# Performance work log

Hardware: AMD Instinct MI355X
Metric: run time of the kernel (lower is better)

The kernel has to match this reference:

```python
import math
import jax, jax.numpy as jnp
import numpy as np

D_MODEL = 1024
N_HEADS = 16
D_FF = 4096
B = 4
T = 1024  # tgt len
S = 1024  # src len
EPS = 1e-6


def _linear_params(key, d_in, d_out):
    kw, kb = jax.random.split(key)
    w = jax.random.normal(kw, (d_out, d_in), dtype=jnp.float32) * 0.02
    b = jax.random.normal(kb, (d_out,), dtype=jnp.float32) * 0.02
    return w, b


def setup_inputs() -> dict:
    key = jax.random.key(0)
    ks = jax.random.split(key, 16)
    x = jax.random.normal(ks[0], (B, T, D_MODEL), dtype=jnp.float32)
    memory = jax.random.normal(ks[1], (B, S, D_MODEL), dtype=jnp.float32)
    # causal [B, T, T] mask (dim==3 branch) and padding [B, S] mask (dim==2 branch)
    tgt_mask = jnp.broadcast_to(jnp.tril(jnp.ones((T, T), dtype=jnp.int32)), (B, T, T))
    src_mask = jnp.ones((B, S), dtype=jnp.int32)
    inp = {"x": x, "memory": memory, "tgt_mask": tgt_mask, "src_mask": src_mask}
    names = ["sa_wq", "sa_wk", "sa_wv", "sa_wo", "ca_wq", "ca_wk", "ca_wv", "ca_wo"]
    for i, n in enumerate(names):
        w, b = _linear_params(ks[2 + i], D_MODEL, D_MODEL)
        inp[n] = w
        inp[n.replace("w", "b")] = b
    inp["ff_w1"], inp["ff_b1"] = _linear_params(ks[10], D_MODEL, D_FF)
    inp["ff_w2"], inp["ff_b2"] = _linear_params(ks[11], D_FF, D_MODEL)
    for i, n in enumerate(["ln1", "ln2", "ln3"]):
        inp[n + "_w"] = jnp.ones((D_MODEL,), dtype=jnp.float32)
        inp[n + "_b"] = jnp.zeros((D_MODEL,), dtype=jnp.float32)
    return inp


def layernorm(x, w, b):
    # torch-faithful: unbiased std (N-1), eps added to std (not variance)
    mean = jnp.mean(x, axis=-1, keepdims=True)
    d = x - mean
    std = jnp.sqrt(jnp.sum(d * d, axis=-1, keepdims=True) / (x.shape[-1] - 1))
    return w * d / (std + EPS) + b


def mha(q_in, kv_in, mask, wq, bq, wk, bk, wv, bv, wo, bo):
    Bb, Tq, D = q_in.shape
    Tk = kv_in.shape[1]
    dk = D // N_HEADS
    if mask.ndim == 2:
        mask4 = mask[:, None, None, :]
    else:
        mask4 = mask[:, None, :, :]
    q = (q_in @ wq.T + bq).reshape(Bb, Tq, N_HEADS, dk).transpose(0, 2, 1, 3)
    k = (kv_in @ wk.T + bk).reshape(Bb, Tk, N_HEADS, dk).transpose(0, 2, 1, 3)
    v = (kv_in @ wv.T + bv).reshape(Bb, Tk, N_HEADS, dk).transpose(0, 2, 1, 3)
    scores = jnp.einsum("bhqd,bhkd->bhqk", q, k) / math.sqrt(dk)
    scores = jnp.where(mask4 == 0, jnp.float32(-1e9), scores)
    attn = jax.nn.softmax(scores, axis=-1)
    out = jnp.einsum("bhqk,bhkd->bhqd", attn, v)
    out = out.transpose(0, 2, 1, 3).reshape(Bb, Tq, D)
    return out @ wo.T + bo


def reference(x, memory, tgt_mask, src_mask,
              sa_wq, sa_bq, sa_wk, sa_bk, sa_wv, sa_bv, sa_wo, sa_bo,
              ca_wq, ca_bq, ca_wk, ca_bk, ca_wv, ca_bv, ca_wo, ca_bo,
              ff_w1, ff_b1, ff_w2, ff_b2,
              ln1_w, ln1_b, ln2_w, ln2_b, ln3_w, ln3_b):
    # pre-norm decoder block (norm_first=True), dropout=0 (eval)
    h = layernorm(x, ln1_w, ln1_b)
    x = x + mha(h, h, tgt_mask, sa_wq, sa_bq, sa_wk, sa_bk, sa_wv, sa_bv, sa_wo, sa_bo)
    h = layernorm(x, ln2_w, ln2_b)
    x = x + mha(h, memory, src_mask, ca_wq, ca_bq, ca_wk, ca_bk, ca_wv, ca_bv, ca_wo, ca_bo)
    h = layernorm(x, ln3_w, ln3_b)
    x = x + (jax.nn.relu(h @ ff_w1.T + ff_b1) @ ff_w2.T + ff_b2)
    return x
```

## Files before the change

kernel.cpp:

```cpp
#include <hip/hip_runtime.h>
#include <hip/hip_bf16.h>

typedef unsigned short u16;
typedef __attribute__((ext_vector_type(4))) float f32x4;
typedef __attribute__((ext_vector_type(8))) short s16x8;
typedef __attribute__((ext_vector_type(4))) short s16x4;
typedef __attribute__((ext_vector_type(8))) __bf16 bf16x8;

#define NTOK 4096
#define DMODEL 1024
#define DFF 4096
#define NH 16
#define TSEQ 1024


__device__ __forceinline__ u16 f2b_hw(float f) {
  union { __bf16 h; u16 u; } cv;
  cv.h = (__bf16)f;
  return cv.u;
}

__device__ __forceinline__ f32x4 mfma16(s16x8 a, s16x8 b, f32x4 c) {
  return __builtin_amdgcn_mfma_f32_16x16x32_bf16((bf16x8)a, (bf16x8)b, c, 0, 0, 0);
}

__device__ __forceinline__ void gload16(const u16* g, u16* l) {
  __builtin_amdgcn_global_load_lds(
      (const __attribute__((address_space(1))) unsigned int*)g,
      (__attribute__((address_space(3))) unsigned int*)l, 16, 0, 0);
}

__device__ __forceinline__ s16x8 ld8s(const u16* t, int row, int eoff) {
  int rx = row & 7;
  const u16* p1 = t + row * 64 + ((((eoff >> 3) ^ rx) << 3) | (eoff & 7));
  const u16* p2 = t + row * 64 + (((((eoff + 16) >> 3) ^ rx) << 3) | (eoff & 7));
  s16x4 lo = *(const s16x4*)p1;
  s16x4 hi = *(const s16x4*)p2;
  s16x8 r;
  r[0] = lo[0]; r[1] = lo[1]; r[2] = lo[2]; r[3] = lo[3];
  r[4] = hi[0]; r[5] = hi[1]; r[6] = hi[2]; r[7] = hi[3];
  return r;
}

__device__ __forceinline__ s16x8 ld16s(const u16* t, int row, int ch) {
  return *(const s16x8*)(t + row * 64 + ((ch ^ (row & 7)) << 3));
}


struct F2B {
  const float* s[11];
  u16* d[11];
};

__global__ __launch_bounds__(256) void f2b_all(F2B a) {
  int bid = blockIdx.x;
  int seg, boff;
  if (bid < 8192) { seg = bid >> 10; boff = bid & 1023; }
  else { int j = bid - 8192; seg = 8 + (j >> 12); boff = j & 4095; }
  size_t i = ((size_t)boff * 256 + threadIdx.x) * 4;
  float4 v = *(const float4*)(a.s[seg] + i);
  ushort4 o = make_ushort4(f2b_hw(v.x), f2b_hw(v.y), f2b_hw(v.z), f2b_hw(v.w));
  *(ushort4*)(a.d[seg] + i) = o;
}


__global__ __launch_bounds__(256) void ln_kernel(const float* __restrict__ x,
                                                 const float* __restrict__ w,
                                                 const float* __restrict__ b,
                                                 u16* __restrict__ out) {
  int row = blockIdx.x;
  int t = threadIdx.x;
  const float* xr = x + (size_t)row * DMODEL;
  float4 v = *(const float4*)(xr + t * 4);
  float s = v.x + v.y + v.z + v.w;
#pragma unroll
  for (int off = 1; off < 64; off <<= 1) s += __shfl_xor(s, off);
  __shared__ float red[8];
  int wid = t >> 6, lane = t & 63;
  if (lane == 0) red[wid] = s;
  __syncthreads();
  float mean = (red[0] + red[1] + red[2] + red[3]) * (1.0f / 1024.0f);
  float dx = v.x - mean, dy = v.y - mean, dz = v.z - mean, dw = v.w - mean;
  float ss = dx * dx + dy * dy + dz * dz + dw * dw;
#pragma unroll
  for (int off = 1; off < 64; off <<= 1) ss += __shfl_xor(ss, off);
  if (lane == 0) red[4 + wid] = ss;
  __syncthreads();
  float sst = red[4] + red[5] + red[6] + red[7];
  float inv = 1.0f / (sqrtf(sst / 1023.0f) + 1e-6f);
  float4 wv = *(const float4*)(w + t * 4);
  float4 bv = *(const float4*)(b + t * 4);
  ushort4 o = make_ushort4(f2b_hw(wv.x * dx * inv + bv.x), f2b_hw(wv.y * dy * inv + bv.y),
                           f2b_hw(wv.z * dz * inv + bv.z), f2b_hw(wv.w * dw * inv + bv.w));
  *(ushort4*)(out + (size_t)row * DMODEL + t * 4) = o;
}


template <int MODE, bool RELU, bool SPLITK = false, int QBUF = -1, int VBUF = -1>
__global__ __launch_bounds__(512) void gemm_bt(const u16* __restrict__ A,
                                               const u16* __restrict__ W,
                                               const float* __restrict__ b0,
                                               const float* __restrict__ b1,
                                               const float* __restrict__ b2,
                                               const float* resid, void* outp,
                                               int M, int N, int K, int ld,
                                               int gx) {
  __shared__ u16 As[2][128 * 64];
  __shared__ u16 Bs[2][128 * 64];
  const int nwg = gridDim.x;
  const int qch = nwg >> 3;
  const int bid = blockIdx.x;
  int wg = (bid & 7) * qch + (bid >> 3);
  int half = 0;
  if (SPLITK) { half = wg & 1; wg >>= 1; }
  const int bx = wg % gx, by = wg / gx;
  const int m0 = by * 128, n0 = bx * 128;
  if (SPLITK) { A += (size_t)half * K; W += (size_t)half * K; }
  const int tid = threadIdx.x;
  const int wid = tid >> 6, lane = tid & 63;
  const int wr = wid >> 2, wc = wid & 3;
  const int lhi = lane >> 4, llo = lane & 15;
  f32x4 acc[4][2] = {};
  const int sr = tid >> 3, sc = tid & 7;
  const int srcoff = (sc ^ (sr & 7)) << 3;

  auto stage = [&](int kk, int buf) {
    const u16* Ap = A + (size_t)(m0 + sr) * ld + kk + srcoff;
    gload16(Ap, &As[buf][tid * 8]);
    gload16(Ap + (size_t)64 * ld, &As[buf][4096 + tid * 8]);
    const u16* Wp = W + (size_t)(n0 + sr) * ld + kk + srcoff;
    gload16(Wp, &Bs[buf][tid * 8]);
    gload16(Wp + (size_t)64 * ld, &Bs[buf][4096 + tid * 8]);
  };

  stage(0, 0);
  __syncthreads();

  for (int k0 = 0; k0 < K; k0 += 64) {
    int cur = (k0 >> 6) & 1;
    if (k0 + 64 < K) stage(k0 + 64, cur ^ 1);
#pragma unroll
    for (int ks8 = 0; ks8 < 8; ks8 += 4) {
      s16x8 af[4], bfr[2];
#pragma unroll
      for (int f = 0; f < 4; f++) af[f] = ld16s(&As[cur][0], wr * 64 + f * 16 + llo, ks8 + lhi);
#pragma unroll
      for (int g = 0; g < 2; g++) bfr[g] = ld16s(&Bs[cur][0], wc * 32 + g * 16 + llo, ks8 + lhi);
#pragma unroll
      for (int f = 0; f < 4; f++)
#pragma unroll
        for (int g = 0; g < 2; g++) acc[f][g] = mfma16(af[f], bfr[g], acc[f][g]);
    }
    __syncthreads();
  }

#pragma unroll
  for (int fm = 0; fm < 4; fm++) {
#pragma unroll
    for (int fn = 0; fn < 2; fn++) {
      int c = n0 + wc * 32 + fn * 16 + llo;
      const int r0 = m0 + wr * 64 + fm * 16 + lhi * 4;
      if (MODE == 2) {
        int buf = c >> 10, cc = c & 1023;
        int hh = cc >> 6, d = cc & 63;
        int bb = r0 >> 10, t0 = r0 & 1023;
        const float* bias = (buf == 0) ? b0 : ((buf == 1) ? b1 : b2);
        float bv = bias[cc];
        float v4[4];
#pragma unroll
        for (int i = 0; i < 4; i++) {
          float v = acc[fm][fn][i] + bv;
          if (buf == QBUF) v *= 0.125f;
          v4[i] = v;
        }
        if (buf == VBUF) {
          ushort4 st = make_ushort4(f2b_hw(v4[0]), f2b_hw(v4[1]), f2b_hw(v4[2]), f2b_hw(v4[3]));
          *(ushort4*)(&((u16*)outp)[(size_t)buf * 4194304 +
                                    (((size_t)(bb * NH + hh)) * 64 + d) * TSEQ + t0]) = st;
        } else {
#pragma unroll
          for (int i = 0; i < 4; i++)
            ((u16*)outp)[(size_t)buf * 4194304 +
                         (((size_t)(bb * NH + hh)) * TSEQ + t0 + i) * 64 + d] = f2b_hw(v4[i]);
        }
      } else {
        float bv = b0 ? b0[c] : 0.0f;
#pragma unroll
        for (int i = 0; i < 4; i++) {
          int r = r0 + i;
          float v = acc[fm][fn][i] + bv;
          if (resid) v += resid[(size_t)r * N + c];
          if (RELU) v = fmaxf(v, 0.0f);
          if (MODE == 0) {
            ((float*)outp)[(size_t)half * M * N + (size_t)r * N + c] = v;
          } else {
            ((u16*)outp)[(size_t)r * N + c] = f2b_hw(v);
          }
        }
      }
    }
  }
}


__global__ __launch_bounds__(256) void ff2_reduce(const float* __restrict__ p,
                                                  const float* __restrict__ bias,
                                                  float* __restrict__ out) {
  int row = blockIdx.x, t = threadIdx.x;
  size_t i = (size_t)row * 1024 + t * 4;
  const float* p1 = p + (size_t)4194304;
  float4 a = *(const float4*)(p + i);
  float4 b = *(const float4*)(p1 + i);
  float4 r = *(const float4*)(out + i);
  float4 bv = *(const float4*)(bias + t * 4);
  float4 o = make_float4(a.x + b.x + r.x + bv.x, a.y + b.y + r.y + bv.y,
                         a.z + b.z + r.z + bv.z, a.w + b.w + r.w + bv.w);
  *(float4*)(out + i) = o;
}


template <bool CAUSAL>
__global__ __launch_bounds__(256) void attn_kernel(const u16* __restrict__ Qg,
                                                   const u16* __restrict__ Kg,
                                                   const u16* __restrict__ Vt,
                                                   u16* __restrict__ Og) {
  const int bid = blockIdx.x;
  const int wg = (bid & 7) * 64 + (bid >> 3);
  const int bh = wg >> 3;
  const int qblk = (wg & 7) ^ (CAUSAL ? 7 * ((bid >> 8) & 1) : 0);
  const int b = bh >> 4, h = bh & 15;
  const int q0 = qblk * 128;
  const int tid = threadIdx.x, wid = tid >> 6, lane = tid & 63;
  const int lhi = lane >> 4, llo = lane & 15;
  __shared__ u16 Ks[2][4096];
  __shared__ u16 Vs[2][4096];

  const int qr = q0 + wid * 16 + llo;
  const u16* qp0 = Qg + ((size_t)bh * TSEQ + qr) * 64;
  s16x8 qf[2][2];
  qf[0][0] = *(const s16x8*)(qp0 + 8 * lhi);
  qf[0][1] = *(const s16x8*)(qp0 + 8 * (4 + lhi));
  qf[1][0] = *(const s16x8*)(qp0 + 4096 + 8 * lhi);
  qf[1][1] = *(const s16x8*)(qp0 + 4096 + 8 * (4 + lhi));

  f32x4 oacc[2][4] = {};
  float mrun[2] = {-1.0e30f, -1.0e30f}, lrun[2] = {0.0f, 0.0f};
  const size_t kvb = (size_t)bh * (TSEQ * 64);
  const int nt = CAUSAL ? ((q0 + 128) >> 6) : (TSEQ >> 6);

  const int srow = tid >> 3;
  const int ssw = ((tid & 7) ^ (srow & 7)) << 3;

  auto stageK = [&](int s0, int buf) {
    const u16* kb = Kg + kvb + (size_t)s0 * 64;
    gload16(kb + (size_t)srow * 64 + ssw, &Ks[buf][tid * 8]);
    gload16(kb + (size_t)(32 + srow) * 64 + ssw, &Ks[buf][2048 + tid * 8]);
  };
  auto stageV = [&](int s0, int buf) {
    const u16* vb2 = Vt + kvb + s0;
    gload16(vb2 + (size_t)srow * TSEQ + ssw, &Vs[buf][tid * 8]);
    gload16(vb2 + (size_t)(32 + srow) * TSEQ + ssw, &Vs[buf][2048 + tid * 8]);
  };

  stageK(0, 0);
  stageV(0, 0);
  __syncthreads();

  for (int t = 0; t < nt; ++t) {
    int cur = t & 1;
    if (t + 1 < nt) {
      stageK((t + 1) * 64, cur ^ 1);
      stageV((t + 1) * 64, cur ^ 1);
    }
    int s0 = t * 64;
    const bool act0 = !CAUSAL || (s0 < q0 + 64);

    s16x8 kf[4][2];
#pragma unroll
    for (int g = 0; g < 4; g++) {
      kf[g][0] = ld16s(&Ks[cur][0], g * 16 + llo, lhi);
      kf[g][1] = ld16s(&Ks[cur][0], g * 16 + llo, 4 + lhi);
    }

    s16x8 pf[2][2];
#pragma unroll
    for (int s = 0; s < 2; s++) {
      if (s == 0 && !act0) continue;
      f32x4 sacc[4] = {};
#pragma unroll
      for (int g = 0; g < 4; g++) {
        sacc[g] = mfma16(kf[g][0], qf[s][0], sacc[g]);
        sacc[g] = mfma16(kf[g][1], qf[s][1], sacc[g]);
      }
      const int qrow = qr + s * 64;
      const bool diag = CAUSAL && (s0 == q0 + s * 64);
      float sv[16];
      float pmax = -1.0e30f;
#pragma unroll
      for (int g = 0; g < 4; g++)
#pragma unroll
        for (int i = 0; i < 4; i++) {
          float sc = sacc[g][i];
          if (diag) {
            int kv = s0 + g * 16 + lhi * 4 + i;
            if (kv > qrow) sc = -1.0e9f;
          }
          sv[g * 4 + i] = sc;
          pmax = fmaxf(pmax, sc);
        }
      pmax = fmaxf(pmax, __shfl_xor(pmax, 16));
      pmax = fmaxf(pmax, __shfl_xor(pmax, 32));
      if (!__all(pmax - mrun[s] <= 8.0f)) {
        float mnew = fmaxf(mrun[s], pmax);
        float alpha = __expf(mrun[s] - mnew);
        lrun[s] *= alpha;
#pragma unroll
        for (int g = 0; g < 4; g++) {
          oacc[s][g][0] *= alpha; oacc[s][g][1] *= alpha;
          oacc[s][g][2] *= alpha; oacc[s][g][3] *= alpha;
        }
        mrun[s] = mnew;
      }
      float ls = 0.0f;
#pragma unroll
      for (int j = 0; j < 16; j++) {
        float p = __expf(sv[j] - mrun[s]);
        ls += p;
        pf[s][j >> 3][((j >> 2) & 1) * 4 + (j & 3)] = (short)f2b_hw(p);
      }
      ls += __shfl_xor(ls, 16);
      ls += __shfl_xor(ls, 32);
      lrun[s] += ls;
    }

#pragma unroll
    for (int dg = 0; dg < 4; dg++) {
      int row = dg * 16 + llo;
      s16x8 vf0 = ld8s(&Vs[cur][0], row, lhi * 4);
      s16x8 vf1 = ld8s(&Vs[cur][0], row, 32 + lhi * 4);
      if (act0) {
        oacc[0][dg] = mfma16(vf0, pf[0][0], oacc[0][dg]);
        oacc[0][dg] = mfma16(vf1, pf[0][1], oacc[0][dg]);
      }
      oacc[1][dg] = mfma16(vf0, pf[1][0], oacc[1][dg]);
      oacc[1][dg] = mfma16(vf1, pf[1][1], oacc[1][dg]);
    }

    __syncthreads();
  }

#pragma unroll
  for (int s = 0; s < 2; s++) {
    float inv = 1.0f / lrun[s];
    u16* orow = Og + (size_t)(b * TSEQ + qr + s * 64) * DMODEL + h * 64;
#pragma unroll
    for (int dg = 0; dg < 4; dg++) {
      ushort4 st = make_ushort4(f2b_hw(oacc[s][dg][0] * inv), f2b_hw(oacc[s][dg][1] * inv),
                                f2b_hw(oacc[s][dg][2] * inv), f2b_hw(oacc[s][dg][3] * inv));
      *(ushort4*)(orow + dg * 16 + lhi * 4) = st;
    }
  }
}


extern "C" void kernel_launch(void* const* d_in, const int* in_sizes, int n_in,
                              void* d_out, int out_size, void* d_ws, size_t ws_size,
                              hipStream_t stream) {
  const float* x      = (const float*)d_in[0];
  const float* memory = (const float*)d_in[1];
  const float* sa_wq = (const float*)d_in[4];  const float* sa_bq = (const float*)d_in[5];
  const float* sa_wk = (const float*)d_in[6];  const float* sa_bk = (const float*)d_in[7];
  const float* sa_wv = (const float*)d_in[8];  const float* sa_bv = (const float*)d_in[9];
  const float* sa_wo = (const float*)d_in[10]; const float* sa_bo = (const float*)d_in[11];
  const float* ca_wq = (const float*)d_in[12]; const float* ca_bq = (const float*)d_in[13];
  const float* ca_wk = (const float*)d_in[14]; const float* ca_bk = (const float*)d_in[15];
  const float* ca_wv = (const float*)d_in[16]; const float* ca_bv = (const float*)d_in[17];
  const float* ca_wo = (const float*)d_in[18]; const float* ca_bo = (const float*)d_in[19];
  const float* ff_w1 = (const float*)d_in[20]; const float* ff_b1 = (const float*)d_in[21];
  const float* ff_w2 = (const float*)d_in[22]; const float* ff_b2 = (const float*)d_in[23];
  const float* ln1_w = (const float*)d_in[24]; const float* ln1_b = (const float*)d_in[25];
  const float* ln2_w = (const float*)d_in[26]; const float* ln2_b = (const float*)d_in[27];
  const float* ln3_w = (const float*)d_in[28]; const float* ln3_b = (const float*)d_in[29];
  float* out = (float*)d_out;

  char* ws = (char*)d_ws;
  const size_t MB = 1u << 20;
  u16* h_bf   = (u16*)(ws + 0 * MB);
  u16* mem_bf = (u16*)(ws + 8 * MB);
  u16* qb     = (u16*)(ws + 16 * MB);
  u16* kb     = (u16*)(ws + 24 * MB);
  u16* vb     = (u16*)(ws + 32 * MB);
  u16* attnb  = (u16*)(ws + 40 * MB);
  u16* ffmid  = (u16*)(ws + 48 * MB);
  float* pk   = (float*)(ws + 16 * MB);
  u16* w_sq   = (u16*)(ws + 80 * MB);
  u16* w_sk   = (u16*)(ws + 82 * MB);
  u16* w_sv   = (u16*)(ws + 84 * MB);
  u16* w_so   = (u16*)(ws + 86 * MB);
  u16* w_cq   = (u16*)(ws + 88 * MB);
  u16* w_ck   = (u16*)(ws + 90 * MB);
  u16* w_cv   = (u16*)(ws + 92 * MB);
  u16* w_co   = (u16*)(ws + 94 * MB);
  u16* w_f1   = (u16*)(ws + 96 * MB);
  u16* w_f2   = (u16*)(ws + 104 * MB);

  F2B fa;
  fa.s[0] = sa_wq; fa.d[0] = w_sq;
  fa.s[1] = sa_wk; fa.d[1] = w_sk;
  fa.s[2] = sa_wv; fa.d[2] = w_sv;
  fa.s[3] = sa_wo; fa.d[3] = w_so;
  fa.s[4] = ca_wq; fa.d[4] = w_cq;
  fa.s[5] = ca_wk; fa.d[5] = w_ck;
  fa.s[6] = ca_wv; fa.d[6] = w_cv;
  fa.s[7] = ca_wo; fa.d[7] = w_co;
  fa.s[8] = ff_w1; fa.d[8] = w_f1;
  fa.s[9] = ff_w2; fa.d[9] = w_f2;
  fa.s[10] = memory; fa.d[10] = mem_bf;
  f2b_all<<<20480, 256, 0, stream>>>(fa);

  ln_kernel<<<4096, 256, 0, stream>>>(x, ln1_w, ln1_b, h_bf);
  gemm_bt<2, false, false, 0, 2><<<768, 512, 0, stream>>>(
      h_bf, w_sq, sa_bq, sa_bk, sa_bv, nullptr, qb, NTOK, 3072, DMODEL, DMODEL, 24);
  attn_kernel<true><<<512, 256, 0, stream>>>(qb, kb, vb, attnb);
  gemm_bt<0, false><<<256, 512, 0, stream>>>(attnb, w_so, sa_bo, nullptr, nullptr,
                                             x, out, NTOK, DMODEL, DMODEL, DMODEL, 8);

  ln_kernel<<<4096, 256, 0, stream>>>(out, ln2_w, ln2_b, h_bf);
  gemm_bt<2, false, false, 0, -1><<<256, 512, 0, stream>>>(
      h_bf, w_cq, ca_bq, nullptr, nullptr, nullptr, qb, NTOK, DMODEL, DMODEL, DMODEL, 8);
  gemm_bt<2, false, false, -1, 1><<<512, 512, 0, stream>>>(
      mem_bf, w_ck, ca_bk, ca_bv, nullptr, nullptr, kb, NTOK, 2048, DMODEL, DMODEL, 16);
  attn_kernel<false><<<512, 256, 0, stream>>>(qb, kb, vb, attnb);
  gemm_bt<0, false><<<256, 512, 0, stream>>>(attnb, w_co, ca_bo, nullptr, nullptr,
                                             out, out, NTOK, DMODEL, DMODEL, DMODEL, 8);

  ln_kernel<<<4096, 256, 0, stream>>>(out, ln3_w, ln3_b, h_bf);
  gemm_bt<1, true><<<1024, 512, 0, stream>>>(h_bf, w_f1, ff_b1, nullptr, nullptr,
                                             nullptr, ffmid, NTOK, DFF, DMODEL, DMODEL, 32);
  gemm_bt<0, false, true><<<512, 512, 0, stream>>>(ffmid, w_f2, nullptr, nullptr, nullptr,
                                                   nullptr, pk, NTOK, DMODEL, 2048, DFF, 8);
  ff2_reduce<<<4096, 256, 0, stream>>>(pk, ff_b2, out);

  (void)in_sizes; (void)n_in; (void)out_size; (void)ws_size;
}
```

Baseline: 330.0 us.

## Add 256x256-tile pipelined GEMM kernel for the FF1 projection

Adds a new GEMM kernel with 256x256 output tiles, double-buffered LDS split into k-halves, and an 8-phase software pipeline. Async global-to-LDS loads are interleaved with MFMA phases, with explicit vmcnt waits, barriers and setprio. The FF1 (ReLU) GEMM now uses it with 256 workgroups instead of 1024 with 128x128 tiles. The goal is more data reuse per tile and better overlap of loads with compute, at the cost of higher register and LDS pressure and fewer workgroups (256 for 256 CUs, one wave of tiles). The epilogue writes scalar bf16 values without vectorization.

```diff
diff --git a/kernel.cpp b/kernel.cpp
--- a/kernel.cpp
+++ b/kernel.cpp
@@ -12,6 +12,8 @@
 #define DFF 4096
 #define NH 16
 #define TSEQ 1024
+
+#define SBAR() do { asm volatile("" ::: "memory"); __builtin_amdgcn_s_barrier(); asm volatile("" ::: "memory"); } while (0)
 
 
 __device__ __forceinline__ u16 f2b_hw(float f) {
@@ -93,6 +95,107 @@
   ushort4 o = make_ushort4(f2b_hw(wv.x * dx * inv + bv.x), f2b_hw(wv.y * dy * inv + bv.y),
                            f2b_hw(wv.z * dz * inv + bv.z), f2b_hw(wv.w * dw * inv + bv.w));
   *(ushort4*)(out + (size_t)row * DMODEL + t * 4) = o;
+}
+
+
+template <bool RELU>
+__global__ __launch_bounds__(512, 2) void gemm256(const u16* __restrict__ A,
+                                                  const u16* __restrict__ W,
+                                                  const float* __restrict__ bias,
+                                                  u16* __restrict__ out,
+                                                  int M, int N, int K, int ld,
+                                                  int gx) {
+  __shared__ u16 As[2][2][8192];
+  __shared__ u16 Bs[2][2][8192];
+  const int nwg = gridDim.x, qch = nwg >> 3, bid = blockIdx.x;
+  const int wg = (bid & 7) * qch + (bid >> 3);
+  const int bx = wg % gx, by = wg / gx;
+  const int m0 = by * 256, n0 = bx * 256;
+  const int tid = threadIdx.x;
+  const int wid = tid >> 6, lane = tid & 63;
+  const int wr = wid >> 2, wc = wid & 3;
+  const int lhi = lane >> 4, llo = lane & 15;
+  f32x4 acc[8][4] = {};
+  const int srow = tid >> 2;
+  const int ssw = ((tid & 3) ^ (srow & 3)) << 3;
+
+  auto unitA = [&](int kt, int kh) {
+    const u16* p = A + (size_t)(m0 + srow) * ld + kt * 64 + kh * 32 + ssw;
+    gload16(p, &As[kt & 1][kh][tid * 8]);
+    gload16(p + (size_t)128 * ld, &As[kt & 1][kh][4096 + tid * 8]);
+  };
+  auto unitB = [&](int kt, int kh) {
+    const u16* p = W + (size_t)(n0 + srow) * ld + kt * 64 + kh * 32 + ssw;
+    gload16(p, &Bs[kt & 1][kh][tid * 8]);
+    gload16(p + (size_t)128 * ld, &Bs[kt & 1][kh][4096 + tid * 8]);
+  };
+
+  s16x8 bf[4];
+  auto phase = [&](int d, int ch, int kh, bool loadB, auto stfn, int vm) {
+    s16x8 af[4];
+#pragma unroll
+    for (int fm = 0; fm < 4; fm++) {
+      int row = wr * 128 + ch * 64 + fm * 16 + llo;
+      af[fm] = *(const s16x8*)(&As[d][kh][row * 32 + ((lhi ^ (row & 3)) << 3)]);
+    }
+    if (loadB) {
+#pragma unroll
+      for (int fn = 0; fn < 4; fn++) {
+        int row = wc * 64 + fn * 16 + llo;
+        bf[fn] = *(const s16x8*)(&Bs[d][kh][row * 32 + ((lhi ^ (row & 3)) << 3)]);
+      }
+    }
+    stfn();
+    SBAR();
+    __builtin_amdgcn_s_setprio(1);
+#pragma unroll
+    for (int fm = 0; fm < 4; fm++)
+#pragma unroll
+      for (int fn = 0; fn < 4; fn++)
+        acc[ch * 4 + fm][fn] = mfma16(af[fm], bf[fn], acc[ch * 4 + fm][fn]);
+    __builtin_amdgcn_s_setprio(0);
+    if (vm == 8) asm volatile("s_waitcnt vmcnt(8)" ::: "memory");
+    else if (vm == 4) asm volatile("s_waitcnt vmcnt(4)" ::: "memory");
+    else if (vm == 0) asm volatile("s_waitcnt vmcnt(0)" ::: "memory");
+    SBAR();
+  };
+
+  unitA(0, 0); unitB(0, 0); unitA(0, 1); unitB(0, 1); unitA(1, 0); unitB(1, 0);
+  asm volatile("s_waitcnt vmcnt(8)" ::: "memory");
+  SBAR();
+
+  const int NPAIR = K >> 7;
+#pragma unroll 1
+  for (int i = 0; i < NPAIR; ++i) {
+    const int tb = 2 * i + 1, tc = 2 * i + 2, td = 2 * i + 3;
+    const bool nx = (i + 1 < NPAIR);
+    phase(0, 0, 0, true,  [&] { unitA(tb, 1); }, -1);
+    phase(0, 1, 0, false, [&] { unitB(tb, 1); }, 8);
+    phase(0, 1, 1, true,  [&] { if (nx) unitA(tc, 0); }, -1);
+    phase(0, 0, 1, false, [&] { if (nx) unitB(tc, 0); }, nx ? 8 : 4);
+    phase(1, 0, 0, true,  [&] { if (nx) unitA(tc, 1); }, -1);
+    phase(1, 1, 0, false, [&] { if (nx) unitB(tc, 1); }, nx ? 8 : 0);
+    phase(1, 1, 1, true,  [&] { if (nx) unitA(td, 0); }, -1);
+    phase(1, 0, 1, false, [&] { if (nx) unitB(td, 0); }, nx ? 8 : -1);
+  }
+
+#pragma unroll
+  for (int ch = 0; ch < 2; ch++)
+#pragma unroll
+    for (int fm = 0; fm < 4; fm++)
+#pragma unroll
+      for (int fn = 0; fn < 4; fn++) {
+        int r0 = m0 + wr * 128 + ch * 64 + fm * 16 + lhi * 4;
+        int c = n0 + wc * 64 + fn * 16 + llo;
+        float bv = bias[c];
+#pragma unroll
+        for (int i2 = 0; i2 < 4; i2++) {
+          float v = acc[ch * 4 + fm][fn][i2] + bv;
+          if (RELU) v = fmaxf(v, 0.0f);
+          out[(size_t)(r0 + i2) * N + c] = f2b_hw(v);
+        }
+      }
+  (void)M;
 }
 
 
@@ -435,8 +538,8 @@
                                              out, out, NTOK, DMODEL, DMODEL, DMODEL, 8);
 
   ln_kernel<<<4096, 256, 0, stream>>>(out, ln3_w, ln3_b, h_bf);
-  gemm_bt<1, true><<<1024, 512, 0, stream>>>(h_bf, w_f1, ff_b1, nullptr, nullptr,
-                                             nullptr, ffmid, NTOK, DFF, DMODEL, DMODEL, 32);
+  gemm256<true><<<256, 512, 0, stream>>>(h_bf, w_f1, ff_b1, ffmid,
+                                         NTOK, DFF, DMODEL, DMODEL, 16);
   gemm_bt<0, false, true><<<512, 512, 0, stream>>>(ffmid, w_f2, nullptr, nullptr, nullptr,
                                                    nullptr, pk, NTOK, DMODEL, 2048, DFF, 8);
   ff2_reduce<<<4096, 256, 0, stream>>>(pk, ff_b2, out);
```

New measurement: 326.6 us. About the same (-1.0%).
